# Kernel optimization log

Measured on AMD Instinct MI355X. Metric: run time of the kernel, lower is better.

Reference implementation:

```python
import jax, jax.numpy as jnp
import numpy as np

B, N, H = 256, 512, 128          # batch of subgraphs, max elements per subgraph, hidden size
NH, DEPTH = 2, 3                 # num_attention_heads (hardcoded 2 in SubGraph), depth
DH = H // NH                     # per-head dim
EPS = 1e-5
NEG = -10000.0


def setup_inputs() -> dict:
    key = jax.random.key(0)
    ks = jax.random.split(key, 12)
    s = 0.02
    x = jax.random.normal(ks[0], (B, N, H), jnp.float32)
    lengths = jax.random.randint(ks[1], (B,), 1, N + 1, jnp.int32)
    # MLP layer_0: Linear + LayerNorm + ReLU
    W0 = jax.random.normal(ks[2], (H, H), jnp.float32) * s
    b0 = jnp.zeros((H,), jnp.float32)
    g0 = jnp.ones((H,), jnp.float32)
    be0 = jnp.zeros((H,), jnp.float32)
    # MLP layer_0_again
    W1 = jax.random.normal(ks[3], (H, H), jnp.float32) * s
    b1 = jnp.zeros((H,), jnp.float32)
    g1 = jnp.ones((H,), jnp.float32)
    be1 = jnp.zeros((H,), jnp.float32)
    # GlobalGraph q/k/v per depth (no output projection in VectorNet GlobalGraph)
    Wq = jax.random.normal(ks[4], (DEPTH, H, H), jnp.float32) * s
    bq = jnp.zeros((DEPTH, H), jnp.float32)
    Wk = jax.random.normal(ks[5], (DEPTH, H, H), jnp.float32) * s
    bk = jnp.zeros((DEPTH, H), jnp.float32)
    Wv = jax.random.normal(ks[6], (DEPTH, H, H), jnp.float32) * s
    bv = jnp.zeros((DEPTH, H), jnp.float32)
    # post-block LayerNorms (layers_2)
    gl = jnp.ones((DEPTH, H), jnp.float32)
    bl = jnp.zeros((DEPTH, H), jnp.float32)
    return dict(hidden_states=x, lengths=lengths, W0=W0, b0=b0, g0=g0, be0=be0,
                W1=W1, b1=b1, g1=g1, be1=be1, Wq=Wq, bq=bq, Wk=Wk, bk=bk,
                Wv=Wv, bv=bv, gl=gl, bl=bl)


def _layer_norm(x, g, b):
    m = jnp.mean(x, axis=-1, keepdims=True)
    v = jnp.mean((x - m) ** 2, axis=-1, keepdims=True)
    return (x - m) * jax.lax.rsqrt(v + EPS) * g + b


def _mlp(x, W, b, g, be):
    return jax.nn.relu(_layer_norm(x @ W + b, g, be))


def reference(hidden_states, lengths, W0, b0, g0, be0, W1, b1, g1, be1,
              Wq, bq, Wk, bk, Wv, bv, gl, bl):
    # vectorized variable-length square mask: mask[i, :len, :len] = 1
    valid = (jnp.arange(N) < lengths[:, None])                      # [B, N] bool
    attn_mask = (valid[:, :, None] & valid[:, None, :]).astype(hidden_states.dtype)  # [B, N, N]
    bias = (1.0 - attn_mask)[:, None, :, :] * NEG                   # [B, 1, N, N]

    h = _mlp(hidden_states, W0, b0, g0, be0)
    h = _mlp(h, W1, b1, g1, be1)

    scale = 1.0 / np.sqrt(DH)
    for d in range(DEPTH):  # small fixed structural loop
        temp = h
        q = (h @ Wq[d] + bq[d]).reshape(B, N, NH, DH)
        k = (h @ Wk[d] + bk[d]).reshape(B, N, NH, DH)
        v = (h @ Wv[d] + bv[d]).reshape(B, N, NH, DH)
        scores = jnp.einsum('bnhd,bmhd->bhnm', q, k) * scale + bias  # [B, NH, N, N]
        probs = jax.nn.softmax(scores, axis=-1)
        ctx = jnp.einsum('bhnm,bmhd->bnhd', probs, v).reshape(B, N, H)
        h = _layer_norm(jax.nn.relu(ctx) + temp, gl[d], bl[d])
    return jnp.max(h, axis=1)  # [B, H]
```

## Files before the change

kernel.cpp:

```cpp
#include <hip/hip_runtime.h>
#include <hip/hip_bf16.h>

#define BB 256
#define NN 512
#define HH 128
#define MM (BB*NN)

typedef unsigned short u16;
typedef unsigned int   u32;
typedef __attribute__((ext_vector_type(8))) short bf16x8;
typedef __attribute__((ext_vector_type(4))) float f32x4;

#define LOG2E  1.4426950408889634f
#define QSCALE (0.125f * LOG2E)
#define NEGB   (-10000.0f * LOG2E)

__device__ __forceinline__ int kswz(int row, int cbyte) {
  return row*128 + (cbyte ^ ((row & 7) << 4));
}
__device__ __forceinline__ int wswz(int row, int cbyte) {
  return row*256 + (cbyte ^ ((row & 7) << 4));
}

__device__ __forceinline__ u16 f2bf(float x) {
  __hip_bfloat16 h = __float2bfloat16(x);
  return *reinterpret_cast<u16*>(&h);
}
__device__ __forceinline__ float bf2f(u16 x) {
  return __uint_as_float(((u32)x) << 16);
}

__device__ __forceinline__ void gld_lds16(const void* g, void* l) {
  __builtin_amdgcn_global_load_lds(
      (__attribute__((address_space(1))) const unsigned int*)g,
      (__attribute__((address_space(3))) unsigned int*)l, 16, 0, 0);
}

__global__ __launch_bounds__(256) void wt_prep(
    const float* __restrict__ W0, const float* __restrict__ W1,
    const float* __restrict__ Wq, const float* __restrict__ Wk,
    const float* __restrict__ Wv, u16* __restrict__ wt)
{
  __shared__ u16 tile[128*128];
  const int t = threadIdx.x;
  const int i = blockIdx.x;
  const float* src;
  if (i == 0) src = W0;
  else if (i == 1) src = W1;
  else {
    const int d = (i-2)/3, which = (i-2)%3;
    src = (which==0 ? Wq : which==1 ? Wk : Wv) + d*HH*HH;
  }
  u16* dst = wt + (size_t)i*HH*HH;

  #pragma unroll
  for (int j = 0; j < 8; j++) {
    const int chunk = t + 256*j;
    const int k = chunk >> 4, c8 = (chunk & 15)*8;
    const float4 a = *(const float4*)&src[k*HH + c8];
    const float4 b = *(const float4*)&src[k*HH + c8 + 4];
    union { u16 s[8]; uint4 v; } u;
    u.s[0]=f2bf(a.x); u.s[1]=f2bf(a.y); u.s[2]=f2bf(a.z); u.s[3]=f2bf(a.w);
    u.s[4]=f2bf(b.x); u.s[5]=f2bf(b.y); u.s[6]=f2bf(b.z); u.s[7]=f2bf(b.w);
    *(uint4*)&tile[k*128 + (((chunk & 15) ^ ((k>>3)&7)) << 3)] = u.v;
  }
  __syncthreads();
  #pragma unroll
  for (int j = 0; j < 8; j++) {
    const int chunk = t + 256*j;
    const int c = chunk >> 4, kb8 = (chunk & 15)*8;
    union { u16 s[8]; uint4 v; } u;
    #pragma unroll
    for (int e = 0; e < 8; e++) {
      const int k = kb8 + e;
      u.s[e] = tile[k*128 + ((((c>>3) ^ ((k>>3)&7)) << 3) | (c & 7))];
    }
    *(uint4*)&dst[c*HH + kb8] = u.v;
  }
}

template<bool F32IN, bool LNRELU>
__device__ __forceinline__ void linear_body(
    const void* __restrict__ Xv, const u16* __restrict__ WT,
    const float* __restrict__ bias, const float* __restrict__ gamma,
    const float* __restrict__ beta, u16* __restrict__ OUT,
    u16* wt_s, u16* xs)
{
  const int t = threadIdx.x;
  const int lane = t & 63, w = t >> 6;
  const int l4 = lane >> 4, l15 = lane & 15;
  const long row0 = (long)blockIdx.x * 128;

  {
    const int rr = lane >> 4;
    const int cb = (lane & 15) * 16;
    #pragma unroll
    for (int i = 0; i < 8; i++) {
      const int seg = w*8 + i;
      const int row = seg*4 + rr;
      gld_lds16((const char*)WT + (size_t)row*256 + (cb ^ ((row & 7) << 4)),
                (char*)wt_s + seg*1024);
    }
    if constexpr (!F32IN) {
      const char* xp = (const char*)((const u16*)Xv + row0*HH);
      #pragma unroll
      for (int i = 0; i < 8; i++) {
        const int seg = w*8 + i;
        const int row = seg*4 + rr;
        gld_lds16(xp + (size_t)row*256 + (cb ^ ((row & 7) << 4)),
                  (char*)xs + seg*1024);
      }
    }
  }
  if constexpr (F32IN) {
    const float* xp = (const float*)Xv + row0*HH;
    #pragma unroll
    for (int i = 0; i < 8; i++) {
      const int chunk = t + 256*i;
      const int r = chunk >> 4, c8 = (chunk & 15)*8;
      const float4 a = *(const float4*)&xp[r*HH + c8];
      const float4 b = *(const float4*)&xp[r*HH + c8 + 4];
      union { u16 s[8]; uint4 v; } u;
      u.s[0]=f2bf(a.x); u.s[1]=f2bf(a.y); u.s[2]=f2bf(a.z); u.s[3]=f2bf(a.w);
      u.s[4]=f2bf(b.x); u.s[5]=f2bf(b.y); u.s[6]=f2bf(b.z); u.s[7]=f2bf(b.w);
      *(uint4*)((char*)xs + wswz(r, c8*2)) = u.v;
    }
  }
  __syncthreads();

  f32x4 acc[2][8];
  #pragma unroll
  for (int m = 0; m < 2; m++)
    #pragma unroll
    for (int n = 0; n < 8; n++)
      { acc[m][n][0]=0.f; acc[m][n][1]=0.f; acc[m][n][2]=0.f; acc[m][n][3]=0.f; }

  #pragma unroll
  for (int ks = 0; ks < 4; ks++) {
    bf16x8 af[2], bf[8];
    #pragma unroll
    for (int m = 0; m < 2; m++)
      af[m] = *(const bf16x8*)((const char*)xs + wswz(w*32 + m*16 + l15, ks*64 + l4*16));
    #pragma unroll
    for (int n = 0; n < 8; n++)
      bf[n] = *(const bf16x8*)((const char*)wt_s + wswz(n*16 + l15, ks*64 + l4*16));
    #pragma unroll
    for (int m = 0; m < 2; m++)
      #pragma unroll
      for (int n = 0; n < 8; n++)
        acc[m][n] = __builtin_amdgcn_mfma_f32_16x16x32_bf16(af[m], bf[n], acc[m][n], 0, 0, 0);
  }

  float bia[8], gam[8], bet[8];
  #pragma unroll
  for (int n = 0; n < 8; n++) {
    bia[n] = bias[n*16 + l15];
    if constexpr (LNRELU) { gam[n] = gamma[n*16 + l15]; bet[n] = beta[n*16 + l15]; }
  }
  #pragma unroll
  for (int m = 0; m < 2; m++) {
    #pragma unroll
    for (int r = 0; r < 4; r++) {
      const long row = row0 + w*32 + m*16 + l4*4 + r;
      float v[8];
      #pragma unroll
      for (int n = 0; n < 8; n++) v[n] = acc[m][n][r] + bia[n];
      if constexpr (LNRELU) {
        float s = 0.f, ss = 0.f;
        #pragma unroll
        for (int n = 0; n < 8; n++) { s += v[n]; ss += v[n]*v[n]; }
        #pragma unroll
        for (int off = 1; off < 16; off <<= 1) {
          s  += __shfl_xor(s,  off);
          ss += __shfl_xor(ss, off);
        }
        const float mean = s * (1.0f/128.0f);
        const float rstd = rsqrtf(ss*(1.0f/128.0f) - mean*mean + 1e-5f);
        #pragma unroll
        for (int n = 0; n < 8; n++)
          v[n] = fmaxf((v[n] - mean)*rstd*gam[n] + bet[n], 0.0f);
      }
      u16* op = OUT + row*HH + l15;
      #pragma unroll
      for (int n = 0; n < 8; n++) op[n*16] = f2bf(v[n]);
    }
  }
}

template<bool F32IN, bool LNRELU>
__global__ __launch_bounds__(256) void linear_mfma(
    const void* __restrict__ Xv, const u16* __restrict__ WT,
    const float* __restrict__ bias, const float* __restrict__ gamma,
    const float* __restrict__ beta, u16* __restrict__ OUT)
{
  __shared__ u16 wt_s[128*128];
  __shared__ u16 xs[128*128];
  linear_body<F32IN, LNRELU>(Xv, WT, bias, gamma, beta, OUT, wt_s, xs);
}

__global__ __launch_bounds__(256) void qkv_mfma(
    const u16* __restrict__ X, const u16* __restrict__ WTd,
    const float* __restrict__ bq, const float* __restrict__ bk,
    const float* __restrict__ bv,
    u16* __restrict__ qb, u16* __restrict__ kb, u16* __restrict__ vb)
{
  __shared__ u16 wt_s[128*128];
  __shared__ u16 xs[128*128];
  const int y = blockIdx.y;
  const u16* WT = WTd + y*HH*HH;
  const float* bias = (y==0) ? bq : (y==1) ? bk : bv;
  u16* OUT = (y==0) ? qb : (y==1) ? kb : vb;
  linear_body<false, false>(X, WT, bias, nullptr, nullptr, OUT, wt_s, xs);
}

__global__ __launch_bounds__(256) void transpose_v_kernel(
    const u16* __restrict__ vb, u16* __restrict__ vT)
{
  __shared__ u16 tile[128*128];
  const int t  = threadIdx.x;
  const int b  = blockIdx.x >> 2;
  const int n0 = (blockIdx.x & 3) * 128;

  #pragma unroll
  for (int i = 0; i < 8; i++) {
    const int chunk = t + 256*i;
    const int n = chunk >> 4, cslot = chunk & 15;
    uint4 d = *(const uint4*)(vb + ((size_t)(b*NN + n0 + n))*HH + cslot*8);
    *(uint4*)&tile[n*128 + ((cslot ^ ((n>>3)&7)) << 3)] = d;
  }
  __syncthreads();
  #pragma unroll
  for (int i = 0; i < 8; i++) {
    const int chunk = t + 256*i;
    const int c = chunk >> 4, nb = (chunk & 15) * 8;
    union { u16 s[8]; uint4 v; } u;
    #pragma unroll
    for (int j = 0; j < 8; j++) {
      const int n = nb + j;
      u.s[j] = tile[n*128 + ((((c>>3) ^ ((n>>3)&7)) << 3) | (c & 7))];
    }
    u16* op = vT + (((size_t)(b*2 + (c>>6)))*64 + (c & 63))*NN + n0 + nb;
    *(uint4*)op = u.v;
  }
}

__global__ __launch_bounds__(256) void attn_kernel(
    const u16* __restrict__ Q, const u16* __restrict__ K,
    const u16* __restrict__ VT, const int* __restrict__ lengths,
    u16* __restrict__ CTX)
{
  __shared__ u16 sh_k[2][64*64];
  __shared__ u16 sh_v[2][64*64];
  __shared__ u16 sh_pq[128*64];
  const int t    = threadIdx.x;
  const int lane = t & 63;
  const int w    = t >> 6;
  const int bid  = blockIdx.x;
  const int qt   = bid & 3;
  const int head = (bid >> 2) & 1;
  const int b    = bid >> 3;
  const int L    = lengths[b];
  const int q0   = qt * 128;
  const int l4 = lane >> 4, l15 = lane & 15;
  const int rr8 = lane >> 3;
  const int cb8 = (lane & 7) * 16;

  const char* qbase  = (const char*)(Q + ((size_t)(b*NN + q0))*HH + head*64);
  const char* kbase0 = (const char*)(K + ((size_t)(b*NN))*HH + head*64);
  const char* vbase0 = (const char*)(VT + (((size_t)(b*2 + head))*64)*NN);

  #pragma unroll
  for (int i = 0; i < 4; i++) {
    const int seg = w*4 + i;
    const int row = seg*8 + rr8;
    gld_lds16(qbase + (size_t)row*256 + (cb8 ^ ((row&7)<<4)),
              (char*)sh_pq + seg*1024);
  }
  #pragma unroll
  for (int i = 0; i < 2; i++) {
    const int seg = w*2 + i;
    const int row = seg*8 + rr8;
    const int sw = cb8 ^ ((row&7)<<4);
    gld_lds16(kbase0 + (size_t)row*256  + sw, (char*)sh_k[0] + seg*1024);
    gld_lds16(vbase0 + (size_t)row*1024 + sw, (char*)sh_v[0] + seg*1024);
  }
  __syncthreads();

  bf16x8 qf[2][2];
  #pragma unroll
  for (int m = 0; m < 2; m++)
    #pragma unroll
    for (int ks = 0; ks < 2; ks++)
      qf[m][ks] = *(const bf16x8*)((const char*)sh_pq +
                    kswz(w*32 + m*16 + l15, ks*64 + l4*16));

  u16* p_lds = sh_pq + w*2048;

  float l_run[2][4];
  f32x4 ctxa[2][4];
  #pragma unroll
  for (int m = 0; m < 2; m++)
    #pragma unroll
    for (int r = 0; r < 4; r++) {
      l_run[m][r] = 0.0f;
      ctxa[m][0][r] = 0.f; ctxa[m][1][r] = 0.f; ctxa[m][2][r] = 0.f; ctxa[m][3][r] = 0.f;
    }

  for (int ch = 0; ch < 8; ch++) {
    const int cur = ch & 1;
    if (ch < 7) {
      const char* kb_ = kbase0 + (size_t)(ch+1)*64*256;
      const char* vb_ = vbase0 + (size_t)(ch+1)*128;
      #pragma unroll
      for (int i = 0; i < 2; i++) {
        const int seg = w*2 + i;
        const int row = seg*8 + rr8;
        const int sw = cb8 ^ ((row&7)<<4);
        gld_lds16(kb_ + (size_t)row*256  + sw, (char*)sh_k[cur^1] + seg*1024);
        gld_lds16(vb_ + (size_t)row*1024 + sw, (char*)sh_v[cur^1] + seg*1024);
      }
    }

    f32x4 acc[2][4];
    #pragma unroll
    for (int m = 0; m < 2; m++)
      #pragma unroll
      for (int n = 0; n < 4; n++)
        { acc[m][n][0]=0.f; acc[m][n][1]=0.f; acc[m][n][2]=0.f; acc[m][n][3]=0.f; }
    #pragma unroll
    for (int ks = 0; ks < 2; ks++) {
      bf16x8 kf[4];
      #pragma unroll
      for (int n = 0; n < 4; n++)
        kf[n] = *(const bf16x8*)((const char*)sh_k[cur] + kswz(n*16 + l15, ks*64 + l4*16));
      #pragma unroll
      for (int m = 0; m < 2; m++)
        #pragma unroll
        for (int n = 0; n < 4; n++)
          acc[m][n] = __builtin_amdgcn_mfma_f32_16x16x32_bf16(
                        qf[m][ks], kf[n], acc[m][n], 0, 0, 0);
    }

    float kb2[4];
    #pragma unroll
    for (int n = 0; n < 4; n++)
      kb2[n] = (ch*64 + n*16 + l15 < L) ? 0.0f : NEGB;

    #pragma unroll
    for (int m = 0; m < 2; m++) {
      #pragma unroll
      for (int r = 0; r < 4; r++) {
        const int  qrow = q0 + w*32 + m*16 + l4*4 + r;
        const bool qv   = qrow < L;
        const float p0 = exp2f(fmaf(acc[m][0][r], QSCALE, qv ? kb2[0] : 0.0f));
        const float p1 = exp2f(fmaf(acc[m][1][r], QSCALE, qv ? kb2[1] : 0.0f));
        const float p2 = exp2f(fmaf(acc[m][2][r], QSCALE, qv ? kb2[2] : 0.0f));
        const float p3 = exp2f(fmaf(acc[m][3][r], QSCALE, qv ? kb2[3] : 0.0f));
        l_run[m][r] += (p0 + p1) + (p2 + p3);
        const int prow = m*16 + l4*4 + r;
        u16* pr = p_lds + prow*64;
        pr[(((0*16 + l15)*2) ^ ((prow&7)<<4)) >> 1] = f2bf(p0);
        pr[(((1*16 + l15)*2) ^ ((prow&7)<<4)) >> 1] = f2bf(p1);
        pr[(((2*16 + l15)*2) ^ ((prow&7)<<4)) >> 1] = f2bf(p2);
        pr[(((3*16 + l15)*2) ^ ((prow&7)<<4)) >> 1] = f2bf(p3);
      }
    }

    #pragma unroll
    for (int ks = 0; ks < 2; ks++) {
      bf16x8 pa[2], vbf[4];
      #pragma unroll
      for (int m = 0; m < 2; m++)
        pa[m] = *(const bf16x8*)((const char*)p_lds + kswz(m*16 + l15, ks*64 + l4*16));
      #pragma unroll
      for (int d = 0; d < 4; d++)
        vbf[d] = *(const bf16x8*)((const char*)sh_v[cur] + kswz(d*16 + l15, ks*64 + l4*16));
      #pragma unroll
      for (int m = 0; m < 2; m++)
        #pragma unroll
        for (int d = 0; d < 4; d++)
          ctxa[m][d] = __builtin_amdgcn_mfma_f32_16x16x32_bf16(
                         pa[m], vbf[d], ctxa[m][d], 0, 0, 0);
    }

    __syncthreads();
  }

  #pragma unroll
  for (int m = 0; m < 2; m++)
    #pragma unroll
    for (int r = 0; r < 4; r++) {
      float lv = l_run[m][r];
      #pragma unroll
      for (int off = 1; off < 16; off <<= 1) lv += __shfl_xor(lv, off);
      const float inv = 1.0f / lv;
      const int qrow = q0 + w*32 + m*16 + l4*4 + r;
      u16* crow = CTX + ((size_t)(b*NN) + qrow)*HH + head*64 + l15;
      crow[0]  = f2bf(ctxa[m][0][r]*inv);
      crow[16] = f2bf(ctxa[m][1][r]*inv);
      crow[32] = f2bf(ctxa[m][2][r]*inv);
      crow[48] = f2bf(ctxa[m][3][r]*inv);
    }
}

__global__ __launch_bounds__(256) void resln_kernel(
    const u16* __restrict__ CTX, u16* Hb,
    const float* __restrict__ gl, const float* __restrict__ bl)
{
  const int t = threadIdx.x;
  const int lane = t & 63;
  const long row = (long)blockIdx.x*4 + (t >> 6);
  const u32 craw = *(const u32*)&CTX[row*HH + lane*2];
  const u32 hraw = *(const u32*)&Hb[row*HH + lane*2];
  const float c0 = bf2f((u16)(craw & 0xffff)), c1 = bf2f((u16)(craw >> 16));
  const float h0 = bf2f((u16)(hraw & 0xffff)), h1 = bf2f((u16)(hraw >> 16));
  const float x0 = fmaxf(c0, 0.0f) + h0;
  const float x1 = fmaxf(c1, 0.0f) + h1;
  float s = x0 + x1, ss = x0*x0 + x1*x1;
  #pragma unroll
  for (int off = 1; off < 64; off <<= 1) {
    s  += __shfl_xor(s,  off);
    ss += __shfl_xor(ss, off);
  }
  const float mean = s * (1.0f/128.0f);
  const float rstd = rsqrtf(ss*(1.0f/128.0f) - mean*mean + 1e-5f);
  const float o0 = (x0 - mean)*rstd*gl[lane*2]   + bl[lane*2];
  const float o1 = (x1 - mean)*rstd*gl[lane*2+1] + bl[lane*2+1];
  *(u32*)&Hb[row*HH + lane*2] = (u32)f2bf(o0) | ((u32)f2bf(o1) << 16);
}

__global__ __launch_bounds__(256) void maxred_kernel(
    const u16* __restrict__ Hb, float* __restrict__ out)
{
  __shared__ float red[256];
  const int b = blockIdx.x;
  const int col = threadIdx.x & 127, half = threadIdx.x >> 7;
  const u16* hp = Hb + ((size_t)b*NN + half*256)*HH + col;
  float m0 = -3.0e38f, m1 = -3.0e38f, m2 = -3.0e38f, m3 = -3.0e38f;
  for (int r = 0; r < 256; r += 4) {
    m0 = fmaxf(m0, bf2f(hp[(r+0)*HH]));
    m1 = fmaxf(m1, bf2f(hp[(r+1)*HH]));
    m2 = fmaxf(m2, bf2f(hp[(r+2)*HH]));
    m3 = fmaxf(m3, bf2f(hp[(r+3)*HH]));
  }
  red[threadIdx.x] = fmaxf(fmaxf(m0, m1), fmaxf(m2, m3));
  __syncthreads();
  if (half == 0) out[(size_t)b*HH + col] = fmaxf(red[col], red[col + 128]);
}

extern "C" void kernel_launch(void* const* d_in, const int* in_sizes, int n_in,
                              void* d_out, int out_size, void* d_ws, size_t ws_size,
                              hipStream_t stream)
{
  const float* x   = (const float*)d_in[0];
  const int* lens  = (const int*)d_in[1];
  const float* W0  = (const float*)d_in[2];
  const float* b0  = (const float*)d_in[3];
  const float* g0  = (const float*)d_in[4];
  const float* be0 = (const float*)d_in[5];
  const float* W1  = (const float*)d_in[6];
  const float* b1  = (const float*)d_in[7];
  const float* g1  = (const float*)d_in[8];
  const float* be1 = (const float*)d_in[9];
  const float* Wq  = (const float*)d_in[10];
  const float* bq  = (const float*)d_in[11];
  const float* Wk  = (const float*)d_in[12];
  const float* bk  = (const float*)d_in[13];
  const float* Wv  = (const float*)d_in[14];
  const float* bv  = (const float*)d_in[15];
  const float* gl  = (const float*)d_in[16];
  const float* bl  = (const float*)d_in[17];
  float* out = (float*)d_out;

  u16* h    = (u16*)d_ws;
  u16* ctxb = h    + (size_t)MM*HH;
  u16* qb   = ctxb + (size_t)MM*HH;
  u16* kb   = qb   + (size_t)MM*HH;
  u16* vb   = kb   + (size_t)MM*HH;
  u16* vT   = vb   + (size_t)MM*HH;
  u16* wt   = vT   + (size_t)MM*HH;

  wt_prep<<<11, 256, 0, stream>>>(W0, W1, Wq, Wk, Wv, wt);

  linear_mfma<true ,true ><<<MM/128, 256, 0, stream>>>(x, wt,           b0, g0, be0, h);
  linear_mfma<false,true ><<<MM/128, 256, 0, stream>>>(h, wt + 1*HH*HH, b1, g1, be1, h);

  for (int d = 0; d < 3; d++) {
    qkv_mfma<<<dim3(MM/128, 3), 256, 0, stream>>>(
        h, wt + (2+3*d)*HH*HH, bq + d*HH, bk + d*HH, bv + d*HH, qb, kb, vb);
    transpose_v_kernel<<<BB*4, 256, 0, stream>>>(vb, vT);
    attn_kernel<<<BB*2*4, 256, 0, stream>>>(qb, kb, vT, lens, ctxb);
    resln_kernel<<<MM/4, 256, 0, stream>>>(ctxb, h, gl + d*HH, bl + d*HH);
  }
  maxred_kernel<<<BB, 256, 0, stream>>>(h, out);
}
```

Before: 619.8 us.

## Rewrite attention with transposed 32x32 MFMA, register-resident P, and masked-chunk skipping

The attention kernel now computes S^T with 32x32x16 MFMAs so each lane owns a query column, which keeps probabilities in registers. They are passed to the PV MFMA via a cross-half lane shuffle instead of a round trip through LDS. It also skips key chunks that are fully padded when all queries in a wave are valid, shortens the chunk loop for fully valid query tiles, and uses an unmasked fast path for the exponentials. Output is written as packed 64-bit stores. This trades LDS traffic and masked work for extra shuffles and more branching.

```diff
diff --git a/kernel.cpp b/kernel.cpp
--- a/kernel.cpp
+++ b/kernel.cpp
@@ -10,6 +10,7 @@
 typedef unsigned int   u32;
 typedef __attribute__((ext_vector_type(8))) short bf16x8;
 typedef __attribute__((ext_vector_type(4))) float f32x4;
+typedef __attribute__((ext_vector_type(16))) float f32x16;
 
 #define LOG2E  1.4426950408889634f
 #define QSCALE (0.125f * LOG2E)
@@ -249,9 +250,9 @@
     const u16* __restrict__ VT, const int* __restrict__ lengths,
     u16* __restrict__ CTX)
 {
+  __shared__ u16 sh_q[128*64];
   __shared__ u16 sh_k[2][64*64];
   __shared__ u16 sh_v[2][64*64];
-  __shared__ u16 sh_pq[128*64];
   const int t    = threadIdx.x;
   const int lane = t & 63;
   const int w    = t >> 6;
@@ -261,9 +262,10 @@
   const int b    = bid >> 3;
   const int L    = lengths[b];
   const int q0   = qt * 128;
-  const int l4 = lane >> 4, l15 = lane & 15;
-  const int rr8 = lane >> 3;
-  const int cb8 = (lane & 7) * 16;
+  const int l31  = lane & 31;
+  const int hi   = lane >> 5;
+  const int rr8  = lane >> 3;
+  const int cb8  = (lane & 7) * 16;
 
   const char* qbase  = (const char*)(Q + ((size_t)(b*NN + q0))*HH + head*64);
   const char* kbase0 = (const char*)(K + ((size_t)(b*NN))*HH + head*64);
@@ -274,7 +276,7 @@
     const int seg = w*4 + i;
     const int row = seg*8 + rr8;
     gld_lds16(qbase + (size_t)row*256 + (cb8 ^ ((row&7)<<4)),
-              (char*)sh_pq + seg*1024);
+              (char*)sh_q + seg*1024);
   }
   #pragma unroll
   for (int i = 0; i < 2; i++) {
@@ -286,29 +288,24 @@
   }
   __syncthreads();
 
-  bf16x8 qf[2][2];
-  #pragma unroll
-  for (int m = 0; m < 2; m++)
-    #pragma unroll
-    for (int ks = 0; ks < 2; ks++)
-      qf[m][ks] = *(const bf16x8*)((const char*)sh_pq +
-                    kswz(w*32 + m*16 + l15, ks*64 + l4*16));
-
-  u16* p_lds = sh_pq + w*2048;
-
-  float l_run[2][4];
-  f32x4 ctxa[2][4];
-  #pragma unroll
-  for (int m = 0; m < 2; m++)
-    #pragma unroll
-    for (int r = 0; r < 4; r++) {
-      l_run[m][r] = 0.0f;
-      ctxa[m][0][r] = 0.f; ctxa[m][1][r] = 0.f; ctxa[m][2][r] = 0.f; ctxa[m][3][r] = 0.f;
-    }
-
-  for (int ch = 0; ch < 8; ch++) {
+  bf16x8 qf[4];
+  #pragma unroll
+  for (int st = 0; st < 4; st++)
+    qf[st] = *(const bf16x8*)((const char*)sh_q + kswz(w*32 + l31, st*32 + hi*16));
+
+  f32x16 cacc[2];
+  #pragma unroll
+  for (int r = 0; r < 16; r++) { cacc[0][r] = 0.f; cacc[1][r] = 0.f; }
+  float l_run = 0.0f;
+
+  const bool q_allv   = (q0 + w*32 + 31) < L;
+  const bool q_allinv = (q0 + w*32) >= L;
+  const bool qv       = (q0 + w*32 + l31) < L;
+  const int  nch      = (q0 + 127 < L) ? ((L + 63) >> 6) : 8;
+
+  for (int ch = 0; ch < nch; ch++) {
     const int cur = ch & 1;
-    if (ch < 7) {
+    if (ch + 1 < nch) {
       const char* kb_ = kbase0 + (size_t)(ch+1)*64*256;
       const char* vb_ = vbase0 + (size_t)(ch+1)*128;
       #pragma unroll
@@ -321,85 +318,91 @@
       }
     }
 
-    f32x4 acc[2][4];
-    #pragma unroll
-    for (int m = 0; m < 2; m++)
-      #pragma unroll
-      for (int n = 0; n < 4; n++)
-        { acc[m][n][0]=0.f; acc[m][n][1]=0.f; acc[m][n][2]=0.f; acc[m][n][3]=0.f; }
-    #pragma unroll
-    for (int ks = 0; ks < 2; ks++) {
-      bf16x8 kf[4];
-      #pragma unroll
-      for (int n = 0; n < 4; n++)
-        kf[n] = *(const bf16x8*)((const char*)sh_k[cur] + kswz(n*16 + l15, ks*64 + l4*16));
-      #pragma unroll
-      for (int m = 0; m < 2; m++)
+    const bool skip = q_allv && (ch*64 >= L);
+    if (!skip) {
+      f32x16 sacc[2];
+      #pragma unroll
+      for (int r = 0; r < 16; r++) { sacc[0][r] = 0.f; sacc[1][r] = 0.f; }
+      #pragma unroll
+      for (int st = 0; st < 4; st++) {
+        const bf16x8 kf0 = *(const bf16x8*)((const char*)sh_k[cur] + kswz(l31,      st*32 + hi*16));
+        const bf16x8 kf1 = *(const bf16x8*)((const char*)sh_k[cur] + kswz(32 + l31, st*32 + hi*16));
+        sacc[0] = __builtin_amdgcn_mfma_f32_32x32x16_bf16(kf0, qf[st], sacc[0], 0, 0, 0);
+        sacc[1] = __builtin_amdgcn_mfma_f32_32x32x16_bf16(kf1, qf[st], sacc[1], 0, 0, 0);
+      }
+
+      const bool fast = (ch*64 + 63 < L) || q_allinv;
+      u32 pw[2][8];
+      #pragma unroll
+      for (int kb2 = 0; kb2 < 2; kb2++) {
+        float p[16];
+        float psum = 0.f;
+        if (fast) {
+          #pragma unroll
+          for (int r = 0; r < 16; r++) {
+            p[r] = exp2f(sacc[kb2][r] * QSCALE);
+            psum += p[r];
+          }
+        } else {
+          #pragma unroll
+          for (int r = 0; r < 16; r++) {
+            const int key = ch*64 + kb2*32 + (r&3) + 8*(r>>2) + 4*hi;
+            const float bias = (qv && key >= L) ? NEGB : 0.0f;
+            p[r] = exp2f(fmaf(sacc[kb2][r], QSCALE, bias));
+            psum += p[r];
+          }
+        }
+        l_run += psum;
         #pragma unroll
-        for (int n = 0; n < 4; n++)
-          acc[m][n] = __builtin_amdgcn_mfma_f32_16x16x32_bf16(
-                        qf[m][ks], kf[n], acc[m][n], 0, 0, 0);
-    }
-
-    float kb2[4];
-    #pragma unroll
-    for (int n = 0; n < 4; n++)
-      kb2[n] = (ch*64 + n*16 + l15 < L) ? 0.0f : NEGB;
-
-    #pragma unroll
-    for (int m = 0; m < 2; m++) {
-      #pragma unroll
-      for (int r = 0; r < 4; r++) {
-        const int  qrow = q0 + w*32 + m*16 + l4*4 + r;
-        const bool qv   = qrow < L;
-        const float p0 = exp2f(fmaf(acc[m][0][r], QSCALE, qv ? kb2[0] : 0.0f));
-        const float p1 = exp2f(fmaf(acc[m][1][r], QSCALE, qv ? kb2[1] : 0.0f));
-        const float p2 = exp2f(fmaf(acc[m][2][r], QSCALE, qv ? kb2[2] : 0.0f));
-        const float p3 = exp2f(fmaf(acc[m][3][r], QSCALE, qv ? kb2[3] : 0.0f));
-        l_run[m][r] += (p0 + p1) + (p2 + p3);
-        const int prow = m*16 + l4*4 + r;
-        u16* pr = p_lds + prow*64;
-        pr[(((0*16 + l15)*2) ^ ((prow&7)<<4)) >> 1] = f2bf(p0);
-        pr[(((1*16 + l15)*2) ^ ((prow&7)<<4)) >> 1] = f2bf(p1);
-        pr[(((2*16 + l15)*2) ^ ((prow&7)<<4)) >> 1] = f2bf(p2);
-        pr[(((3*16 + l15)*2) ^ ((prow&7)<<4)) >> 1] = f2bf(p3);
-      }
-    }
-
-    #pragma unroll
-    for (int ks = 0; ks < 2; ks++) {
-      bf16x8 pa[2], vbf[4];
-      #pragma unroll
-      for (int m = 0; m < 2; m++)
-        pa[m] = *(const bf16x8*)((const char*)p_lds + kswz(m*16 + l15, ks*64 + l4*16));
-      #pragma unroll
-      for (int d = 0; d < 4; d++)
-        vbf[d] = *(const bf16x8*)((const char*)sh_v[cur] + kswz(d*16 + l15, ks*64 + l4*16));
-      #pragma unroll
-      for (int m = 0; m < 2; m++)
+        for (int mm = 0; mm < 4; mm++)
+          #pragma unroll
+          for (int e = 0; e < 2; e++)
+            pw[kb2][mm*2+e] = (u32)f2bf(p[4*mm+2*e]) | ((u32)f2bf(p[4*mm+2*e+1]) << 16);
+      }
+
+      #pragma unroll
+      for (int kb2 = 0; kb2 < 2; kb2++) {
         #pragma unroll
-        for (int d = 0; d < 4; d++)
-          ctxa[m][d] = __builtin_amdgcn_mfma_f32_16x16x32_bf16(
-                         pa[m], vbf[d], ctxa[m][d], 0, 0, 0);
+        for (int st = 0; st < 2; st++) {
+          const u32 w00 = pw[kb2][(2*st+0)*2+0], w01 = pw[kb2][(2*st+0)*2+1];
+          const u32 w10 = pw[kb2][(2*st+1)*2+0], w11 = pw[kb2][(2*st+1)*2+1];
+          const u32 own0 = hi ? w10 : w00;
+          const u32 own1 = hi ? w11 : w01;
+          const u32 snd0 = hi ? w00 : w10;
+          const u32 snd1 = hi ? w01 : w11;
+          const u32 rcv0 = (u32)__shfl_xor((int)snd0, 32);
+          const u32 rcv1 = (u32)__shfl_xor((int)snd1, 32);
+          union { u32 u[4]; bf16x8 v; } pb;
+          pb.u[0] = hi ? rcv0 : own0;
+          pb.u[1] = hi ? rcv1 : own1;
+          pb.u[2] = hi ? own0 : rcv0;
+          pb.u[3] = hi ? own1 : rcv1;
+          #pragma unroll
+          for (int db = 0; db < 2; db++) {
+            const bf16x8 vf = *(const bf16x8*)((const char*)sh_v[cur] +
+                                kswz(db*32 + l31, kb2*64 + st*32 + hi*16));
+            cacc[db] = __builtin_amdgcn_mfma_f32_32x32x16_bf16(vf, pb.v, cacc[db], 0, 0, 0);
+          }
+        }
+      }
     }
 
     __syncthreads();
   }
 
-  #pragma unroll
-  for (int m = 0; m < 2; m++)
-    #pragma unroll
-    for (int r = 0; r < 4; r++) {
-      float lv = l_run[m][r];
-      #pragma unroll
-      for (int off = 1; off < 16; off <<= 1) lv += __shfl_xor(lv, off);
-      const float inv = 1.0f / lv;
-      const int qrow = q0 + w*32 + m*16 + l4*4 + r;
-      u16* crow = CTX + ((size_t)(b*NN) + qrow)*HH + head*64 + l15;
-      crow[0]  = f2bf(ctxa[m][0][r]*inv);
-      crow[16] = f2bf(ctxa[m][1][r]*inv);
-      crow[32] = f2bf(ctxa[m][2][r]*inv);
-      crow[48] = f2bf(ctxa[m][3][r]*inv);
+  const float l_full = l_run + __shfl_xor(l_run, 32);
+  const float inv = 1.0f / l_full;
+  const int qrow = q0 + w*32 + l31;
+  u16* crow = CTX + ((size_t)(b*NN) + qrow)*HH + head*64;
+  #pragma unroll
+  for (int db = 0; db < 2; db++)
+    #pragma unroll
+    for (int mm = 0; mm < 4; mm++) {
+      const int dh0 = db*32 + mm*8 + hi*4;
+      uint2 o;
+      o.x = (u32)f2bf(cacc[db][4*mm+0]*inv) | ((u32)f2bf(cacc[db][4*mm+1]*inv) << 16);
+      o.y = (u32)f2bf(cacc[db][4*mm+2]*inv) | ((u32)f2bf(cacc[db][4*mm+3]*inv) << 16);
+      *(uint2*)(crow + dh0) = o;
     }
 }
 
```

New measurement: 578.5 us. -6.7%, faster.
